# Performance work log

Hardware: AMD Instinct MI355X
Metric: run time of the kernel (lower is better)

The kernel has to match this reference:

```python
import jax, jax.numpy as jnp
import numpy as np

N, E = 100000, 1600000
IN_F, H, D = 128, 4, 32
NEG_SLOPE = 0.2


def setup_inputs() -> dict:
    key = jax.random.key(0)
    k1, k2, k3, k4, k5, k6 = jax.random.split(key, 6)
    feat = jax.random.normal(k1, (N, IN_F), dtype=jnp.float32)
    src = jax.random.randint(k2, (E,), 0, N, dtype=jnp.int32)
    dst = jax.random.randint(k3, (E,), 0, N, dtype=jnp.int32)
    # learned params (xavier-ish scale)
    W = jax.random.normal(k4, (IN_F, H * D), dtype=jnp.float32) * (2.0 / (IN_F + H * D)) ** 0.5
    attn_l = jax.random.normal(k5, (H, D), dtype=jnp.float32) * 0.1
    attn_r = jax.random.normal(k6, (H, D), dtype=jnp.float32) * 0.1
    return {"feat": feat, "W": W, "attn_l": attn_l, "attn_r": attn_r, "src": src, "dst": dst}


def reference(feat, W, attn_l, attn_r, src, dst):
    n = feat.shape[0]
    # linear projection: [N, H, D]
    ft = (feat @ W).reshape(n, H, D)
    # per-node attention logits: [N, H]
    el = jnp.einsum('nhd,hd->nh', ft, attn_l)
    er = jnp.einsum('nhd,hd->nh', ft, attn_r)
    # per-edge score e_ij = LeakyReLU(el[src] + er[dst]): [E, H]
    e = el[src] + er[dst]
    e = jnp.where(e > 0, e, NEG_SLOPE * e)
    # edge softmax over incoming edges of each destination node
    emax = jax.ops.segment_max(e, dst, num_segments=n)        # [N, H]
    emax = jnp.where(jnp.isfinite(emax), emax, 0.0)           # guard isolated nodes
    ex = jnp.exp(e - emax[dst])                               # [E, H]
    denom = jax.ops.segment_sum(ex, dst, num_segments=n)      # [N, H]
    denom = jnp.where(denom > 0, denom, 1.0)
    a = ex / denom[dst]                                       # [E, H]
    # weighted gather-scatter aggregation: sum_j a_ij * ft_j
    m = ft[src] * a[:, :, None]                               # [E, H, D]
    rst = jax.ops.segment_sum(m, dst, num_segments=n)         # [N, H, D]
    return rst
```

## Files before the change

### kernel.cpp

```cpp
#include <hip/hip_runtime.h>
#include <hip/hip_fp16.h>

constexpr int IN_F = 128;
constexpr int NH   = 4;
constexpr int ND   = 32;
constexpr int HD   = 128;
constexpr float NEG_SLOPE = 0.2f;
constexpr int NBLK   = 256;
constexpr int BSH    = 7;
constexpr int BNODES = 1 << BSH;

using short8 = __attribute__((ext_vector_type(8))) short;
using f32x4  = __attribute__((ext_vector_type(4))) float;
using f32x2  = __attribute__((ext_vector_type(2))) float;

__device__ inline unsigned bf16b(float f) {
  unsigned u = __float_as_uint(f);
  return (u + 0x7FFFu + ((u >> 16) & 1u)) >> 16;
}

__global__ __launch_bounds__(256) void k_chist(
    const int* __restrict__ dst, int* __restrict__ cnt, int ne, int nbuk,
    const float* __restrict__ W, const float* __restrict__ attn_l,
    const float* __restrict__ attn_r, unsigned* __restrict__ wtx) {
  const int t = threadIdx.x;
  const int item = blockIdx.x * 256 + t;
  if (item < 144 * 16) {
    const int r = item >> 4, s = item & 15;
    const int k0 = s * 8;
    unsigned pk[4];
    if (r < HD) {
#pragma unroll
      for (int j2 = 0; j2 < 4; ++j2) {
        const unsigned lo = bf16b(W[(size_t)(k0 + 2 * j2) * HD + r]);
        const unsigned hi = bf16b(W[(size_t)(k0 + 2 * j2 + 1) * HD + r]);
        pk[j2] = lo | (hi << 16);
      }
    } else if (r < HD + 8) {
      const int j8 = r - HD;
      const int h = j8 & 3;
      const float* av = (j8 < 4 ? attn_l : attn_r) + h * ND;
      float sums[8];
#pragma unroll
      for (int j = 0; j < 8; ++j) {
        const float4* wv = (const float4*)&W[(size_t)(k0 + j) * HD + h * ND];
        const float4* a4 = (const float4*)av;
        float sum = 0.f;
#pragma unroll
        for (int c4 = 0; c4 < ND / 4; ++c4) {
          const float4 w = wv[c4], a = a4[c4];
          sum += w.x * a.x + w.y * a.y + w.z * a.z + w.w * a.w;
        }
        sums[j] = sum;
      }
#pragma unroll
      for (int j2 = 0; j2 < 4; ++j2)
        pk[j2] = bf16b(sums[2 * j2]) | (bf16b(sums[2 * j2 + 1]) << 16);
    } else {
      pk[0] = pk[1] = pk[2] = pk[3] = 0;
    }
    *(uint4*)&wtx[r * 64 + ((s ^ (r & 7)) << 2)] =
        make_uint4(pk[0], pk[1], pk[2], pk[3]);
  }
  __shared__ int hist[1024];
  for (int b = t; b < nbuk; b += 256) hist[b] = 0;
  __syncthreads();
  const int chunk = (ne + NBLK - 1) / NBLK;
  const int start = blockIdx.x * chunk;
  const int end = min(start + chunk, ne);
  for (int e = start + t; e < end; e += 256)
    atomicAdd(&hist[dst[e] >> BSH], 1);
  __syncthreads();
  for (int b = t; b < nbuk; b += 256) cnt[b * NBLK + blockIdx.x] = hist[b];
}

__global__ __launch_bounds__(256) void k_scan1(
    const int* __restrict__ in, int* __restrict__ pexcl,
    int* __restrict__ bsum, int len) {
  const int t = threadIdx.x;
  const int base = blockIdx.x * 1024 + t * 4;
  int v0 = base + 0 < len ? in[base + 0] : 0;
  int v1 = base + 1 < len ? in[base + 1] : 0;
  int v2 = base + 2 < len ? in[base + 2] : 0;
  int v3 = base + 3 < len ? in[base + 3] : 0;
  const int s = v0 + v1 + v2 + v3;
  const int lane = t & 63, w = t >> 6;
  int x = s;
#pragma unroll
  for (int off = 1; off < 64; off <<= 1) {
    int y = __shfl_up(x, off);
    if (lane >= off) x += y;
  }
  __shared__ int ws[4];
  if (lane == 63) ws[w] = x;
  __syncthreads();
  int woff = 0;
  for (int i = 0; i < w; ++i) woff += ws[i];
  int run = woff + x - s;
  if (base + 0 < len) { pexcl[base + 0] = run; run += v0; }
  if (base + 1 < len) { pexcl[base + 1] = run; run += v1; }
  if (base + 2 < len) { pexcl[base + 2] = run; run += v2; }
  if (base + 3 < len) { pexcl[base + 3] = run; run += v3; }
  if (t == 0) bsum[blockIdx.x] = ws[0] + ws[1] + ws[2] + ws[3];
}

__global__ __launch_bounds__(256) void k_scan23(
    const int* __restrict__ pexcl, const int* __restrict__ bsum,
    int* __restrict__ outv, int B, int len) {
  const int t = threadIdx.x;
  const int s = t < B ? bsum[t] : 0;
  const int lane = t & 63, w = t >> 6;
  int x = s;
#pragma unroll
  for (int off = 1; off < 64; off <<= 1) {
    int y = __shfl_up(x, off);
    if (lane >= off) x += y;
  }
  __shared__ int ws[4];
  __shared__ int sboff[256];
  if (lane == 63) ws[w] = x;
  __syncthreads();
  int woff = 0;
  for (int i = 0; i < w; ++i) woff += ws[i];
  sboff[t] = woff + x - s;
  __syncthreads();
  const int myoff = sboff[blockIdx.x];
  const int base = blockIdx.x * 1024 + t * 4;
#pragma unroll
  for (int j = 0; j < 4; ++j)
    if (base + j < len) outv[base + j] = pexcl[base + j] + myoff;
}

__global__ __launch_bounds__(256) void k_gemm(
    const float* __restrict__ feat, const unsigned* __restrict__ wtx,
    unsigned* __restrict__ ftb2, float* __restrict__ el, float* __restrict__ er,
    int n, const int* __restrict__ src, const int* __restrict__ dst,
    const int* __restrict__ scanned, unsigned* __restrict__ pairp,
    int ne, int nbuk) {
  __shared__ unsigned sB[144 * 64];
  __shared__ int cur[1024];
  const int t = threadIdx.x;
  {
    const uint4* wx = (const uint4*)wtx;
    uint4* sx = (uint4*)sB;
    for (int it = t; it < 144 * 16; it += 256) sx[it] = wx[it];
  }
  __syncthreads();

  const int lane = t & 63;
  const int wv   = t >> 6;
  const int r0   = blockIdx.x * 128 + wv * 32;
  const int lrow = lane & 15;
  const int lk   = lane >> 4;

  if (r0 < n) {
    f32x4 acc[2][9];
#pragma unroll
    for (int st = 0; st < 2; ++st)
#pragma unroll
      for (int ct = 0; ct < 9; ++ct) acc[st][ct] = (f32x4)0.f;

#pragma unroll
    for (int ks = 0; ks < 4; ++ks) {
      short8 b[9];
#pragma unroll
      for (int ct = 0; ct < 9; ++ct) {
        const int row = ct * 16 + lrow;
        const int slot = ks * 4 + lk;
        b[ct] = *(const short8*)&sB[row * 64 + ((slot ^ (row & 7)) << 2)];
      }
#pragma unroll
      for (int st = 0; st < 2; ++st) {
        int arow = r0 + st * 16 + lrow;
        arow = arow < n ? arow : n - 1;
        const float* ap = feat + (size_t)arow * IN_F + ks * 32 + lk * 8;
        const float4 f0 = *(const float4*)ap;
        const float4 f1 = *(const float4*)(ap + 4);
        short8 a;
        a[0] = (short)bf16b(f0.x); a[1] = (short)bf16b(f0.y);
        a[2] = (short)bf16b(f0.z); a[3] = (short)bf16b(f0.w);
        a[4] = (short)bf16b(f1.x); a[5] = (short)bf16b(f1.y);
        a[6] = (short)bf16b(f1.z); a[7] = (short)bf16b(f1.w);
#pragma unroll
        for (int ct = 0; ct < 9; ++ct)
          acc[st][ct] = __builtin_amdgcn_mfma_f32_16x16x32_bf16(a, b[ct], acc[st][ct], 0, 0, 0);
      }
    }

#pragma unroll
    for (int st = 0; st < 2; ++st) {
#pragma unroll
      for (int i = 0; i < 4; ++i) {
        const int r = r0 + st * 16 + lk * 4 + i;
        if (r >= n) continue;
#pragma unroll
        for (int ct = 0; ct < 4; ++ct) {
          const unsigned pk = bf16b(acc[st][ct][i]) | (bf16b(acc[st][ct + 4][i]) << 16);
          ftb2[(size_t)r * 64 + ct * 16 + lrow] = pk;
        }
        if (lrow < 4)      el[r * NH + lrow]     = acc[st][8][i];
        else if (lrow < 8) er[r * NH + lrow - 4] = acc[st][8][i];
      }
    }
  }

  if (blockIdx.x < NBLK) {
    for (int b = t; b < nbuk; b += 256) cur[b] = scanned[b * NBLK + blockIdx.x];
    __syncthreads();
    const int chunk = (ne + NBLK - 1) / NBLK;
    const int start = blockIdx.x * chunk;
    const int end = min(start + chunk, ne);
    for (int e = start + t; e < end; e += 256) {
      const int d = dst[e];
      const int pos = atomicAdd(&cur[d >> BSH], 1);
      pairp[pos] = ((unsigned)src[e] << BSH) | (unsigned)(d & (BNODES - 1));
    }
  }
}

__global__ __launch_bounds__(256) void k_fsort(
    const unsigned* __restrict__ pair, const int* __restrict__ scanned,
    const float* __restrict__ el, const float* __restrict__ er,
    int* __restrict__ offsets, int4* __restrict__ rec,
    int n, int ne, int nbuk) {
  const int b = blockIdx.x;
  const int t = threadIdx.x;
  const int base = scanned[b * NBLK];
  const int endp = (b + 1 < nbuk) ? scanned[(b + 1) * NBLK] : ne;
  __shared__ int hist[BNODES];
  __shared__ int cur[BNODES];
  __shared__ int ws2[2];
  if (t < BNODES) hist[t] = 0;
  __syncthreads();
  for (int i = base + t; i < endp; i += 256)
    atomicAdd(&hist[pair[i] & (BNODES - 1)], 1);
  __syncthreads();
  int x = 0, v = 0;
  if (t < BNODES) {
    v = hist[t];
    x = v;
    const int lane = t & 63;
#pragma unroll
    for (int off = 1; off < 64; off <<= 1) {
      int y = __shfl_up(x, off);
      if (lane >= off) x += y;
    }
    if (lane == 63) ws2[t >> 6] = x;
  }
  __syncthreads();
  if (t < BNODES) {
    if (t >= 64) x += ws2[0];
    const int excl = base + x - v;
    cur[t] = excl;
    const int node = (b << BSH) + t;
    if (node < n) offsets[node] = excl;
  }
  if (b == 0 && t == 0) offsets[n] = ne;
  __syncthreads();
  for (int i = base + t; i < endp; i += 256) {
    const unsigned pr = pair[i];
    const int s = (int)(pr >> BSH);
    const int fn = (int)(pr & (BNODES - 1));
    const int d = (b << BSH) + fn;
    const int pos = atomicAdd(&cur[fn], 1);
    const float4 l = *(const float4*)(el + (size_t)s * NH);
    const float4 r = *(const float4*)(er + (size_t)d * NH);
    float e0 = l.x + r.x, e1 = l.y + r.y, e2 = l.z + r.z, e3 = l.w + r.w;
    e0 = e0 > 0.f ? e0 : NEG_SLOPE * e0;
    e1 = e1 > 0.f ? e1 : NEG_SLOPE * e1;
    e2 = e2 > 0.f ? e2 : NEG_SLOPE * e2;
    e3 = e3 > 0.f ? e3 : NEG_SLOPE * e3;
    const __half2 h02 = __float22half2_rn(make_float2(__expf(e0), __expf(e2)));
    const __half2 h13 = __float22half2_rn(make_float2(__expf(e1), __expf(e3)));
    int4 rc;
    rc.x = s;
    rc.y = *(const int*)&h02;
    rc.z = s;
    rc.w = *(const int*)&h13;
    rec[pos] = rc;
  }
}

__global__ __launch_bounds__(256) void k_aggr(
    const int* __restrict__ offsets, const int* __restrict__ rec,
    const unsigned* __restrict__ ftb2, float* __restrict__ out, int n) {
  const int t = threadIdx.x;
  const int lane = t & 63;
  const int gw = (blockIdx.x * 256 + t) >> 6;
  const int q = lane >> 4;
  const int c = lane & 15;
  const int hsel = c >> 3;
  const int node = gw * 4 + q;
  int start = 0, end = 0;
  if (node < n) { start = offsets[node]; end = offsets[node + 1]; }
  const char* recb = (const char*)rec + (hsel << 3);
  const unsigned* fb = ftb2 + (c << 2);

  f32x2 acc0 = {0.f, 0.f}, acc1 = {0.f, 0.f};
  f32x2 acc2 = {0.f, 0.f}, acc3 = {0.f, 0.f};
  f32x2 den  = {0.f, 0.f};

  for (int i = start; i < end; i += 4) {
    int2 r[4];
#pragma unroll
    for (int k = 0; k < 4; ++k) {
      const int idx = i + k;
      const int cl = min(idx, end - 1);
      r[k] = *(const int2*)(recb + ((size_t)cl << 4));
      if (idx >= end) r[k].y = 0;
    }
#pragma unroll
    for (int k = 0; k < 4; ++k) {
      const uint4 v = *(const uint4*)(fb + (size_t)r[k].x * 64);
      const float2 pf = __half22float2(*(const __half2*)&r[k].y);
      f32x2 p; p.x = pf.x; p.y = pf.y;
      f32x2 f;
      f.x = __uint_as_float(v.x << 16);
      f.y = __uint_as_float(v.x & 0xFFFF0000u);
      asm("v_pk_fma_f32 %0, %1, %2, %0" : "+v"(acc0) : "v"(f), "v"(p));
      f.x = __uint_as_float(v.y << 16);
      f.y = __uint_as_float(v.y & 0xFFFF0000u);
      asm("v_pk_fma_f32 %0, %1, %2, %0" : "+v"(acc1) : "v"(f), "v"(p));
      f.x = __uint_as_float(v.z << 16);
      f.y = __uint_as_float(v.z & 0xFFFF0000u);
      asm("v_pk_fma_f32 %0, %1, %2, %0" : "+v"(acc2) : "v"(f), "v"(p));
      f.x = __uint_as_float(v.w << 16);
      f.y = __uint_as_float(v.w & 0xFFFF0000u);
      asm("v_pk_fma_f32 %0, %1, %2, %0" : "+v"(acc3) : "v"(f), "v"(p));
      asm("v_pk_add_f32 %0, %1, %0" : "+v"(den) : "v"(p));
    }
  }

  if (node < n) {
    const float d0 = den.x > 0.f ? den.x : 1.f;
    const float d1 = den.y > 0.f ? den.y : 1.f;
    const float r0 = __builtin_amdgcn_rcpf(d0);
    const float r1 = __builtin_amdgcn_rcpf(d1);
    float* orow = out + (size_t)node * HD;
    *(float4*)(orow + (c << 2)) =
        make_float4(acc0.x * r0, acc1.x * r0, acc2.x * r0, acc3.x * r0);
    *(float4*)(orow + 64 + (c << 2)) =
        make_float4(acc0.y * r1, acc1.y * r1, acc2.y * r1, acc3.y * r1);
  }
}

extern "C" void kernel_launch(void* const* d_in, const int* in_sizes, int n_in,
                              void* d_out, int out_size, void* d_ws, size_t ws_size,
                              hipStream_t stream) {
  const float* feat   = (const float*)d_in[0];
  const float* W      = (const float*)d_in[1];
  const float* attn_l = (const float*)d_in[2];
  const float* attn_r = (const float*)d_in[3];
  const int*   src    = (const int*)d_in[4];
  const int*   dst    = (const int*)d_in[5];
  const int n  = in_sizes[0] / IN_F;
  const int ne = in_sizes[4];
  float* out = (float*)d_out;

  const int nbuk = (n + BNODES - 1) >> BSH;
  const int tbl  = nbuk * NBLK;
  const int Bt   = (tbl + 1023) / 1024;

  char* wp = (char*)d_ws;
  unsigned* ftb2 = (unsigned*)wp; wp += (size_t)n * 64 * 4;
  int4*  rec     = (int4*)wp;     wp += (size_t)ne * 16;
  unsigned* pairp = (unsigned*)wp; wp += (size_t)ne * 4;
  unsigned* wtx  = (unsigned*)wp; wp += (size_t)144 * 64 * 4;
  float* el      = (float*)wp;    wp += (size_t)n * NH * 4;
  float* er      = (float*)wp;    wp += (size_t)n * NH * 4;
  int*   cnt     = (int*)wp;      wp += (size_t)tbl * 4;
  int*   pexcl   = (int*)wp;      wp += (size_t)tbl * 4;
  int*   scanned = (int*)wp;      wp += (size_t)tbl * 4;
  int*   offsets = (int*)wp;      wp += (size_t)(n + 1) * 4;
  int*   bsum    = (int*)wp;      wp += 256 * 4;

  k_chist<<<NBLK, 256, 0, stream>>>(dst, cnt, ne, nbuk, W, attn_l, attn_r, wtx);
  k_scan1<<<Bt, 256, 0, stream>>>(cnt, pexcl, bsum, tbl);
  k_scan23<<<Bt, 256, 0, stream>>>(pexcl, bsum, scanned, Bt, tbl);
  k_gemm<<<(n + 127) / 128, 256, 0, stream>>>(feat, wtx, ftb2, el, er, n,
                                              src, dst, scanned, pairp, ne, nbuk);
  k_fsort<<<nbuk, 256, 0, stream>>>(pairp, scanned, el, er, offsets, rec, n, ne, nbuk);
  k_aggr<<<(n + 15) / 16, 256, 0, stream>>>(offsets, (const int*)rec, ftb2, out, n);
}
```

Baseline: 144.4 us.

## Fuse per-bucket edge sort with aggregation, keeping edge records in LDS

```diff
diff --git a/kernel.cpp b/kernel.cpp
--- a/kernel.cpp
+++ b/kernel.cpp
@@ -9,6 +9,7 @@
 constexpr int NBLK   = 256;
 constexpr int BSH    = 7;
 constexpr int BNODES = 1 << BSH;
+constexpr int CAP    = 2560;
 
 using short8 = __attribute__((ext_vector_type(8))) short;
 using f32x4  = __attribute__((ext_vector_type(4))) float;
@@ -218,18 +219,22 @@
   }
 }
 
-__global__ __launch_bounds__(256) void k_fsort(
+__global__ __launch_bounds__(256) void k_fsagg(
     const unsigned* __restrict__ pair, const int* __restrict__ scanned,
     const float* __restrict__ el, const float* __restrict__ er,
-    int* __restrict__ offsets, int4* __restrict__ rec,
-    int n, int ne, int nbuk) {
+    const unsigned* __restrict__ ftb2, float* __restrict__ out,
+    int4* __restrict__ spill, int n, int ne, int nbuk) {
   const int b = blockIdx.x;
   const int t = threadIdx.x;
   const int base = scanned[b * NBLK];
   const int endp = (b + 1 < nbuk) ? scanned[(b + 1) * NBLK] : ne;
+  const bool spl = (endp - base) > CAP;
   __shared__ int hist[BNODES];
   __shared__ int cur[BNODES];
   __shared__ int ws2[2];
+  __shared__ int s_src[CAP];
+  __shared__ int2 s_h[CAP];
+
   if (t < BNODES) hist[t] = 0;
   __syncthreads();
   for (int i = base + t; i < endp; i += 256)
@@ -250,13 +255,10 @@
   __syncthreads();
   if (t < BNODES) {
     if (t >= 64) x += ws2[0];
-    const int excl = base + x - v;
-    cur[t] = excl;
-    const int node = (b << BSH) + t;
-    if (node < n) offsets[node] = excl;
-  }
-  if (b == 0 && t == 0) offsets[n] = ne;
-  __syncthreads();
+    cur[t] = x - v;
+  }
+  __syncthreads();
+
   for (int i = base + t; i < endp; i += 256) {
     const unsigned pr = pair[i];
     const int s = (int)(pr >> BSH);
@@ -272,76 +274,97 @@
     e3 = e3 > 0.f ? e3 : NEG_SLOPE * e3;
     const __half2 h02 = __float22half2_rn(make_float2(__expf(e0), __expf(e2)));
     const __half2 h13 = __float22half2_rn(make_float2(__expf(e1), __expf(e3)));
-    int4 rc;
-    rc.x = s;
-    rc.y = *(const int*)&h02;
-    rc.z = s;
-    rc.w = *(const int*)&h13;
-    rec[pos] = rc;
-  }
-}
-
-__global__ __launch_bounds__(256) void k_aggr(
-    const int* __restrict__ offsets, const int* __restrict__ rec,
-    const unsigned* __restrict__ ftb2, float* __restrict__ out, int n) {
-  const int t = threadIdx.x;
+    const int h02i = *(const int*)&h02;
+    const int h13i = *(const int*)&h13;
+    if (!spl) {
+      s_src[pos] = s;
+      s_h[pos] = make_int2(h02i, h13i);
+    } else {
+      spill[(size_t)base + pos] = make_int4(s, h02i, s, h13i);
+    }
+  }
+  __syncthreads();
+
   const int lane = t & 63;
-  const int gw = (blockIdx.x * 256 + t) >> 6;
+  const int wv = t >> 6;
   const int q = lane >> 4;
   const int c = lane & 15;
   const int hsel = c >> 3;
-  const int node = gw * 4 + q;
-  int start = 0, end = 0;
-  if (node < n) { start = offsets[node]; end = offsets[node + 1]; }
-  const char* recb = (const char*)rec + (hsel << 3);
   const unsigned* fb = ftb2 + (c << 2);
-
-  f32x2 acc0 = {0.f, 0.f}, acc1 = {0.f, 0.f};
-  f32x2 acc2 = {0.f, 0.f}, acc3 = {0.f, 0.f};
-  f32x2 den  = {0.f, 0.f};
-
-  for (int i = start; i < end; i += 4) {
-    int2 r[4];
-#pragma unroll
-    for (int k = 0; k < 4; ++k) {
-      const int idx = i + k;
-      const int cl = min(idx, end - 1);
-      r[k] = *(const int2*)(recb + ((size_t)cl << 4));
-      if (idx >= end) r[k].y = 0;
-    }
-#pragma unroll
-    for (int k = 0; k < 4; ++k) {
-      const uint4 v = *(const uint4*)(fb + (size_t)r[k].x * 64);
-      const float2 pf = __half22float2(*(const __half2*)&r[k].y);
-      f32x2 p; p.x = pf.x; p.y = pf.y;
-      f32x2 f;
-      f.x = __uint_as_float(v.x << 16);
-      f.y = __uint_as_float(v.x & 0xFFFF0000u);
-      asm("v_pk_fma_f32 %0, %1, %2, %0" : "+v"(acc0) : "v"(f), "v"(p));
-      f.x = __uint_as_float(v.y << 16);
-      f.y = __uint_as_float(v.y & 0xFFFF0000u);
-      asm("v_pk_fma_f32 %0, %1, %2, %0" : "+v"(acc1) : "v"(f), "v"(p));
-      f.x = __uint_as_float(v.z << 16);
-      f.y = __uint_as_float(v.z & 0xFFFF0000u);
-      asm("v_pk_fma_f32 %0, %1, %2, %0" : "+v"(acc2) : "v"(f), "v"(p));
-      f.x = __uint_as_float(v.w << 16);
-      f.y = __uint_as_float(v.w & 0xFFFF0000u);
-      asm("v_pk_fma_f32 %0, %1, %2, %0" : "+v"(acc3) : "v"(f), "v"(p));
-      asm("v_pk_add_f32 %0, %1, %0" : "+v"(den) : "v"(p));
-    }
-  }
-
-  if (node < n) {
-    const float d0 = den.x > 0.f ? den.x : 1.f;
-    const float d1 = den.y > 0.f ? den.y : 1.f;
-    const float r0 = __builtin_amdgcn_rcpf(d0);
-    const float r1 = __builtin_amdgcn_rcpf(d1);
-    float* orow = out + (size_t)node * HD;
-    *(float4*)(orow + (c << 2)) =
-        make_float4(acc0.x * r0, acc1.x * r0, acc2.x * r0, acc3.x * r0);
-    *(float4*)(orow + 64 + (c << 2)) =
-        make_float4(acc0.y * r1, acc1.y * r1, acc2.y * r1, acc3.y * r1);
-  }
+  const int* sh = (const int*)s_h;
+
+#define PKSTEP(SRCI, HV)                                              \
+  {                                                                   \
+    const uint4 vv = *(const uint4*)(fb + (size_t)(SRCI) * 64);       \
+    const float2 pf = __half22float2(*(const __half2*)&(HV));         \
+    f32x2 p; p.x = pf.x; p.y = pf.y;                                  \
+    f32x2 f;                                                          \
+    f.x = __uint_as_float(vv.x << 16);                                \
+    f.y = __uint_as_float(vv.x & 0xFFFF0000u);                        \
+    asm("v_pk_fma_f32 %0, %1, %2, %0" : "+v"(acc0) : "v"(f), "v"(p)); \
+    f.x = __uint_as_float(vv.y << 16);                                \
+    f.y = __uint_as_float(vv.y & 0xFFFF0000u);                        \
+    asm("v_pk_fma_f32 %0, %1, %2, %0" : "+v"(acc1) : "v"(f), "v"(p)); \
+    f.x = __uint_as_float(vv.z << 16);                                \
+    f.y = __uint_as_float(vv.z & 0xFFFF0000u);                        \
+    asm("v_pk_fma_f32 %0, %1, %2, %0" : "+v"(acc2) : "v"(f), "v"(p)); \
+    f.x = __uint_as_float(vv.w << 16);                                \
+    f.y = __uint_as_float(vv.w & 0xFFFF0000u);                        \
+    asm("v_pk_fma_f32 %0, %1, %2, %0" : "+v"(acc3) : "v"(f), "v"(p)); \
+    asm("v_pk_add_f32 %0, %1, %0" : "+v"(den) : "v"(p));              \
+  }
+
+  for (int pass = 0; pass < BNODES / 16; ++pass) {
+    const int fn = pass * 16 + wv * 4 + q;
+    const int node = (b << BSH) + fn;
+    const int endl = cur[fn];
+    const int startl = endl - hist[fn];
+    f32x2 acc0 = {0.f, 0.f}, acc1 = {0.f, 0.f};
+    f32x2 acc2 = {0.f, 0.f}, acc3 = {0.f, 0.f};
+    f32x2 den  = {0.f, 0.f};
+
+    if (!spl) {
+      for (int i = startl; i < endl; i += 4) {
+        int sidx[4], hv[4];
+#pragma unroll
+        for (int k = 0; k < 4; ++k) {
+          const int idx = min(i + k, endl - 1);
+          sidx[k] = s_src[idx];
+          hv[k] = sh[idx * 2 + hsel];
+          if (i + k >= endl) hv[k] = 0;
+        }
+#pragma unroll
+        for (int k = 0; k < 4; ++k) PKSTEP(sidx[k], hv[k])
+      }
+    } else {
+      const char* recb = (const char*)spill + (hsel << 3);
+      const int gs = base + startl, ge = base + endl;
+      for (int i = gs; i < ge; i += 4) {
+        int2 r[4];
+#pragma unroll
+        for (int k = 0; k < 4; ++k) {
+          const int idx = min(i + k, ge - 1);
+          r[k] = *(const int2*)(recb + ((size_t)idx << 4));
+          if (i + k >= ge) r[k].y = 0;
+        }
+#pragma unroll
+        for (int k = 0; k < 4; ++k) PKSTEP(r[k].x, r[k].y)
+      }
+    }
+
+    if (node < n) {
+      const float d0 = den.x > 0.f ? den.x : 1.f;
+      const float d1 = den.y > 0.f ? den.y : 1.f;
+      const float r0 = __builtin_amdgcn_rcpf(d0);
+      const float r1 = __builtin_amdgcn_rcpf(d1);
+      float* orow = out + (size_t)node * HD;
+      *(float4*)(orow + (c << 2)) =
+          make_float4(acc0.x * r0, acc1.x * r0, acc2.x * r0, acc3.x * r0);
+      *(float4*)(orow + 64 + (c << 2)) =
+          make_float4(acc0.y * r1, acc1.y * r1, acc2.y * r1, acc3.y * r1);
+    }
+  }
+#undef PKSTEP
 }
 
 extern "C" void kernel_launch(void* const* d_in, const int* in_sizes, int n_in,
@@ -362,23 +385,22 @@
   const int Bt   = (tbl + 1023) / 1024;
 
   char* wp = (char*)d_ws;
-  unsigned* ftb2 = (unsigned*)wp; wp += (size_t)n * 64 * 4;
-  int4*  rec     = (int4*)wp;     wp += (size_t)ne * 16;
+  unsigned* ftb2  = (unsigned*)wp; wp += (size_t)n * 64 * 4;
+  int4*  spill    = (int4*)wp;     wp += (size_t)ne * 16;
   unsigned* pairp = (unsigned*)wp; wp += (size_t)ne * 4;
-  unsigned* wtx  = (unsigned*)wp; wp += (size_t)144 * 64 * 4;
-  float* el      = (float*)wp;    wp += (size_t)n * NH * 4;
-  float* er      = (float*)wp;    wp += (size_t)n * NH * 4;
-  int*   cnt     = (int*)wp;      wp += (size_t)tbl * 4;
-  int*   pexcl   = (int*)wp;      wp += (size_t)tbl * 4;
-  int*   scanned = (int*)wp;      wp += (size_t)tbl * 4;
-  int*   offsets = (int*)wp;      wp += (size_t)(n + 1) * 4;
-  int*   bsum    = (int*)wp;      wp += 256 * 4;
+  unsigned* wtx   = (unsigned*)wp; wp += (size_t)144 * 64 * 4;
+  float* el       = (float*)wp;    wp += (size_t)n * NH * 4;
+  float* er       = (float*)wp;    wp += (size_t)n * NH * 4;
+  int*   cnt      = (int*)wp;      wp += (size_t)tbl * 4;
+  int*   pexcl    = (int*)wp;      wp += (size_t)tbl * 4;
+  int*   scanned  = (int*)wp;      wp += (size_t)tbl * 4;
+  int*   bsum     = (int*)wp;      wp += 256 * 4;
 
   k_chist<<<NBLK, 256, 0, stream>>>(dst, cnt, ne, nbuk, W, attn_l, attn_r, wtx);
   k_scan1<<<Bt, 256, 0, stream>>>(cnt, pexcl, bsum, tbl);
   k_scan23<<<Bt, 256, 0, stream>>>(pexcl, bsum, scanned, Bt, tbl);
   k_gemm<<<(n + 127) / 128, 256, 0, stream>>>(feat, wtx, ftb2, el, er, n,
                                               src, dst, scanned, pairp, ne, nbuk);
-  k_fsort<<<nbuk, 256, 0, stream>>>(pairp, scanned, el, er, offsets, rec, n, ne, nbuk);
-  k_aggr<<<(n + 15) / 16, 256, 0, stream>>>(offsets, (const int*)rec, ftb2, out, n);
-}
+  k_fsagg<<<nbuk, 256, 0, stream>>>(pairp, scanned, el, er, ftb2, out,
+                                    spill, n, ne, nbuk);
+}
```

Measured after the change: 133.5 us. 7.5% less time.
